# Kernel optimization log

Measured on AMD Instinct MI355X. Metric: run time of the kernel, lower is better.

The kernel has to match this reference:

```python
import jax, jax.numpy as jnp
import numpy as np

N = 8192
F_IN = 512
F_OUT = 256
NEG_SLOPE = 0.01  # F.leaky_relu default
MASK_VAL = -1000000000000000.0


def setup_inputs() -> dict:
    key = jax.random.key(0)
    k1, k2, k3, k4 = jax.random.split(key, 4)
    stdv = 1.0 / np.sqrt(F_OUT)
    x = jax.random.normal(k1, (N, F_IN), dtype=jnp.float32)
    weight = jax.random.uniform(k2, (F_IN, F_OUT), dtype=jnp.float32, minval=-stdv, maxval=stdv)
    att_vec = jax.random.normal(k3, (2 * F_OUT, 1), dtype=jnp.float32) * 0.05
    adj = jax.random.randint(k4, (N, N), 0, 2, dtype=jnp.int32)
    return {"x": x, "weight": weight, "att_vec": att_vec, "adj": adj}


def _pair_indices(n):
    # Reproduces the (buggy-but-faithful) torch.cat(dim=0).view(n,-1,2f) indexing:
    # element (i,j,:f)  = out[idx(2m)], element (i,j,f:) = out[idx(2m+1)], m = i*n+j
    # idx(r) = r // n if r < n*n else (r - n*n) % n
    nn_ = n * n
    m = jnp.arange(nn_, dtype=jnp.int32)
    r0 = 2 * m
    r1 = r0 + 1
    idx1 = jnp.where(r0 < nn_, r0 // n, (r0 - nn_) % n)
    idx2 = jnp.where(r1 < nn_, r1 // n, (r1 - nn_) % n)
    return idx1, idx2


def reference(x, weight, att_vec, adj):
    n = x.shape[0]
    f = weight.shape[1]
    # dropout p=0.0 -> identity
    out = x @ weight                      # (n, f)
    a1 = att_vec[:f, 0]                   # (f,)
    a2 = att_vec[f:, 0]                   # (f,)
    s1 = out @ a1                         # (n,)
    s2 = out @ a2                         # (n,)
    idx1, idx2 = _pair_indices(n)
    scores = (s1[idx1] + s2[idx2]).reshape(n, n)
    scores = jax.nn.leaky_relu(scores, NEG_SLOPE)
    scores = jnp.where(adj > 0, scores, MASK_VAL)
    attn = jax.nn.softmax(scores, axis=1)  # F.softmax default dim=1 for 2D
    return jax.nn.sigmoid(attn @ out)      # (n, f)
```

## Files before the change

### kernel.cpp

```cpp
#include <hip/hip_runtime.h>

using u32 = unsigned int;
using u16 = unsigned short;

typedef __attribute__((ext_vector_type(8)))  __bf16 bf16x8;
typedef __attribute__((ext_vector_type(16))) float  f32x16;
typedef __attribute__((ext_vector_type(4)))  float  f32x4;
typedef __attribute__((ext_vector_type(4)))  int    i32x4;

__device__ __forceinline__ u32 f2bf(float f){
  u32 u = __float_as_uint(f);
  return (u + 0x7FFFu + ((u >> 16) & 1u)) >> 16;
}
__device__ __forceinline__ u32 pack2bf(float lo, float hi){
  return f2bf(lo) | (f2bf(hi) << 16);
}
__device__ __forceinline__ float bfu2f(u32 us){ return __uint_as_float(us << 16); }
__device__ __forceinline__ float lrelu(float x){ return x > 0.f ? x : 0.01f * x; }

__global__ void k0_wt(const float* __restrict__ w, u16* __restrict__ wT){
  int u = blockIdx.x * 256 + threadIdx.x;
  int k = u >> 8, n = u & 255;
  wT[(size_t)n * 512 + k] = (u16)f2bf(w[(size_t)k * 256 + n]);
}

__global__ __launch_bounds__(512, 2) void k1_gemm(const float* __restrict__ x,
    const u16* __restrict__ wT, const float* __restrict__ av, u16* __restrict__ outF,
    float* __restrict__ v0, float* __restrict__ v1, u16* __restrict__ pbf){
  __shared__ float tb[8][32][36];
  __shared__ float afl[512];
  __shared__ float sred[2][32][17];
  __shared__ float srw[2][32];
  const int i0 = blockIdx.x * 32;
  const int tid = threadIdx.x;
  const int lane = tid & 63, wv = tid >> 6;
  const int r = lane & 31, h = lane >> 5;
  const float* xp = x + (size_t)(i0 + r) * 512 + h * 8;
  const u16*   bp = wT + (size_t)(wv * 32 + r) * 512 + h * 8;
  f32x16 acc = {};
  for (int s = 0; s < 32; ++s){
    f32x4 a0 = *(const f32x4*)xp;
    f32x4 a1 = *(const f32x4*)(xp + 4);
    i32x4 pk = { (int)pack2bf(a0[0], a0[1]), (int)pack2bf(a0[2], a0[3]),
                 (int)pack2bf(a1[0], a1[1]), (int)pack2bf(a1[2], a1[3]) };
    bf16x8 af = __builtin_bit_cast(bf16x8, pk);
    bf16x8 bf = *(const bf16x8*)bp;
    acc = __builtin_amdgcn_mfma_f32_32x32x16_bf16(af, bf, acc, 0, 0, 0);
    xp += 16; bp += 16;
  }
  #pragma unroll
  for (int re = 0; re < 16; ++re){
    int rr = (re & 3) + 8 * (re >> 2) + 4 * h;
    tb[wv][r][rr] = acc[re];
  }
  afl[tid] = av[tid];
  __syncthreads();
  {
    const int n2 = lane >> 1, ic = (lane & 1) * 16;
    const float* tp = &tb[wv][n2][ic];
    i32x4 w0 = { (int)pack2bf(tp[0],tp[1]),   (int)pack2bf(tp[2],tp[3]),
                 (int)pack2bf(tp[4],tp[5]),   (int)pack2bf(tp[6],tp[7]) };
    i32x4 w1 = { (int)pack2bf(tp[8],tp[9]),   (int)pack2bf(tp[10],tp[11]),
                 (int)pack2bf(tp[12],tp[13]), (int)pack2bf(tp[14],tp[15]) };
    const int n = wv * 32 + n2;
    const int k16 = (i0 + ic) >> 4;
    u16* op = outF + ((size_t)k16 * 256 + n) * 16;
    *(i32x4*)op = w0;
    *((i32x4*)op + 1) = w1;
  }
  const int row = tid & 31, g = tid >> 5;
  const int w8 = g >> 1, fh = (g & 1) * 16;
  float a1c = 0.f, a2c = 0.f;
  #pragma unroll
  for (int f = 0; f < 16; ++f){
    float tv = tb[w8][fh + f][row];
    a1c = fmaf(tv, afl[w8 * 32 + fh + f], a1c);
    a2c = fmaf(tv, afl[256 + w8 * 32 + fh + f], a2c);
  }
  sred[0][row][g] = a1c; sred[1][row][g] = a2c;
  __syncthreads();
  if (tid < 64){
    int which = tid >> 5, r2 = tid & 31;
    float s = 0.f;
    #pragma unroll
    for (int g2 = 0; g2 < 16; ++g2) s += sred[which][r2][g2];
    srw[which][r2] = s;
  }
  __syncthreads();
  if (tid < 16){
    int k = (i0 >> 1) + tid;
    float sa  = srw[0][2*tid],   sb  = srw[1][2*tid];
    float sa1 = srw[0][2*tid+1], sb1 = srw[1][2*tid+1];
    v0[k] = lrelu(sa + sb);
    v1[k] = lrelu(sa1 + sb1);
    float w = lrelu(sa + sb1);
    pbf[k] = (u16)f2bf(__expf(w));
  }
}

__global__ __launch_bounds__(512, 2) void k3_main(const int* __restrict__ adj,
    const u16* __restrict__ outF, const u16* __restrict__ pbf,
    float* __restrict__ P, float* __restrict__ pd){
  __shared__ u16 AbS[2][16896];
  __shared__ u32 plS[2048];
  __shared__ float dshS[32];
  const int bid = blockIdx.x;
  const int xcd = bid & 7, slot = bid >> 3;
  const int c = xcd & 1;
  const int tile = (xcd >> 1) * 64 + slot;
  const bool top = tile < 128;
  const int i0 = tile * 32;
  const int pb = tile * 2 + c;
  const int tid = threadIdx.x, l = tid & 63, w = tid >> 6;
  const int r = l & 31, h = l >> 5;
  const int fb = w * 32;
  const int* aq0 = adj + (size_t)(i0 + w) * 8192 + c * 4096 + l * 4;
  const u16* bq0 = outF + (size_t)c * 1048576 + (fb + r) * 16 + h * 8;

  if (top){
    plS[tid] = 0x3F803F80u; plS[tid + 512] = 0x3F803F80u;
    plS[tid + 1024] = 0x3F803F80u; plS[tid + 1536] = 0x3F803F80u;
  } else {
    const u32* ps = (const u32*)pbf;
    plS[tid] = ps[tid]; plS[tid + 512] = ps[tid + 512];
    plS[tid + 1024] = ps[tid + 1024]; plS[tid + 1536] = ps[tid + 1536];
  }
  __syncthreads();

  i32x4 ar[8];
  bf16x8 BA[4], BB[4];
  f32x16 acc = {};
  float d4[4] = {0.f, 0.f, 0.f, 0.f};

#define ADJ_H(HF_,PH_) { \
  _Pragma("unroll") for (int j_ = 0; j_ < 2; ++j_){ \
    const int q_ = (HF_) * 2 + j_; \
    const int* ap_ = aq0 + q_ * 65536 + (PH_) * 512; \
    ar[q_*2]   = *(const i32x4*)ap_; \
    ar[q_*2+1] = *(const i32x4*)(ap_ + 256); } \
  asm volatile("" ::: "memory"); }

#define B_ISS4(B_,G_) { const u16* bb_ = bq0 + (size_t)(G_) * 4096; \
  B_[0] = *(const bf16x8*)bb_;            B_[1] = *(const bf16x8*)(bb_ + 4096); \
  B_[2] = *(const bf16x8*)(bb_ + 8192);   B_[3] = *(const bf16x8*)(bb_ + 12288); \
  asm volatile("" ::: "memory"); }

#define MFMA4(B_,RB_,S_) { \
  __builtin_amdgcn_s_setprio(1); \
  _Pragma("unroll") for (int j_ = 0; j_ < 4; ++j_){ \
    bf16x8 a_ = *(const bf16x8*)((RB_) + ((S_) * 4 + j_) * 528 + r * 16 + h * 8); \
    acc = __builtin_amdgcn_mfma_f32_32x32x16_bf16(a_, B_[j_], acc, 0, 0, 0); } \
  __builtin_amdgcn_s_setprio(0); }

#define PACK(PH_,WB_) { \
  _Pragma("unroll") for (int q_ = 0; q_ < 4; ++q_){ \
    const int row_ = q_ * 8 + w; \
    _Pragma("unroll") for (int L_ = 0; L_ < 2; ++L_){ \
      i32x4 a_ = ar[q_*2 + L_]; \
      uint2 pp_ = *(const uint2*)(plS + (((PH_) & 7) * 256 + L_ * 128 + 2 * l)); \
      u32 w0_ = ((((u32)(-a_[0])) & 0xFFFFu) | (((u32)(-a_[1])) << 16)) & pp_.x; \
      u32 w1_ = ((((u32)(-a_[2])) & 0xFFFFu) | (((u32)(-a_[3])) << 16)) & pp_.y; \
      d4[q_] += __uint_as_float(w0_ << 16) + __uint_as_float(w0_ & 0xFFFF0000u) \
              + __uint_as_float(w1_ << 16) + __uint_as_float(w1_ & 0xFFFF0000u); \
      const int slot_ = L_ * 16 + (l >> 2); \
      uint2 wv_; wv_.x = w0_; wv_.y = w1_; \
      *(uint2*)((WB_) + slot_ * 528 + row_ * 16 + (l & 3) * 4) = wv_; } } }

#define KBAR() { asm volatile("s_waitcnt lgkmcnt(0)" ::: "memory"); \
  __builtin_amdgcn_s_barrier(); asm volatile("" ::: "memory"); }

  ADJ_H(0, 0); ADJ_H(1, 0);
  B_ISS4(BA, 0);
  PACK(0, &AbS[0][0]);
  KBAR();

  #pragma unroll 1
  for (int t = 0; t < 8; ++t){
    const u16* rb = &AbS[t & 1][0];
    u16* wb = &AbS[(t + 1) & 1][0];
    #pragma unroll
    for (int s = 0; s < 8; ++s){
      if (!(t == 7 && s == 7)){
        const int g = t * 32 + (s + 1) * 4;
        if (s & 1){ B_ISS4(BA, g); } else { B_ISS4(BB, g); }
      }
      if (t < 7 && s == 0) ADJ_H(0, t + 1);
      if (t < 7 && s == 1) ADJ_H(1, t + 1);
      if (s & 1){ MFMA4(BB, rb, s); } else { MFMA4(BA, rb, s); }
    }
    if (t < 7){
      PACK(t + 1, wb);
      KBAR();
    }
  }

#undef ADJ_H
#undef B_ISS4
#undef MFMA4
#undef PACK
#undef KBAR

  #pragma unroll
  for (int q = 0; q < 4; ++q){
    float v = d4[q];
    #pragma unroll
    for (int mk = 1; mk < 64; mk <<= 1) v += __shfl_xor(v, mk);
    if (l == 0) dshS[q * 8 + w] = v;
  }
  __syncthreads();
  if (tid < 32) pd[(size_t)pb * 32 + tid] = dshS[tid];
  float* Pb = P + (size_t)pb * 8192 + fb + r;
  #pragma unroll
  for (int e = 0; e < 16; ++e){
    int rr = (e & 3) + 8 * (e >> 2) + 4 * h;
    __builtin_nontemporal_store(acc[e], Pb + (size_t)rr * 256);
  }
}

__global__ void k4_final(const float* __restrict__ P, const float* __restrict__ pd,
    const float* __restrict__ v0, const float* __restrict__ v1, float* __restrict__ out){
  const int i = blockIdx.x, n = threadIdx.x;
  const int tile = i >> 5, rloc = i & 31;
  const size_t base = (size_t)tile * 16384 + (size_t)rloc * 256 + n;
  float P0 = __builtin_nontemporal_load(P + base);
  float P1 = __builtin_nontemporal_load(P + base + 8192);
  float d0 = pd[tile * 64 + rloc];
  float d1 = pd[tile * 64 + 32 + rloc];
  float val;
  if (i < 4096){
    float va = v0[i], vb = v1[i];
    float m = fmaxf(va, vb);
    float e0 = __expf(va - m), e1 = __expf(vb - m);
    val = (e0 * P0 + e1 * P1) / (e0 * d0 + e1 * d1);
  } else {
    val = (P0 + P1) / (d0 + d1);
  }
  out[(size_t)i * 256 + n] = 1.0f / (1.0f + __expf(-val));
}

extern "C" void kernel_launch(void* const* d_in, const int* in_sizes, int n_in,
                              void* d_out, int out_size, void* d_ws, size_t ws_size,
                              hipStream_t stream)
{
  const float* x      = (const float*)d_in[0];
  const float* weight = (const float*)d_in[1];
  const float* av     = (const float*)d_in[2];
  const int*   adj    = (const int*)d_in[3];
  float* out = (float*)d_out;
  char* ws = (char*)d_ws;
  float* P     = (float*)(ws + 0);
  float* pd    = (float*)(ws + 16777216);
  u16*   outF  = (u16*)  (ws + 16842752);
  u16*   wT    = (u16*)  (ws + 21037056);
  u16*   pbf   = (u16*)  (ws + 21299200);
  float* v0    = (float*)(ws + 21307392);
  float* v1    = (float*)(ws + 21323776);

  k0_wt    <<<512, 256, 0, stream>>>(weight, wT);
  k1_gemm  <<<256, 512, 0, stream>>>(x, wT, av, outF, v0, v1, pbf);
  k3_main  <<<512, 512, 0, stream>>>(adj, outF, pbf, P, pd);
  k4_final <<<8192, 256, 0, stream>>>(P, pd, v0, v1, out);
}
```

Baseline: 115.6 us.

## Warp-specialize attention kernel into adj producers and MFMA consumers with 64-row tiles

Splits each k3_main block into four producer waves that load and pack adjacency masks into LDS and four consumer waves that stream outF and run MFMAs. The row tile doubles to 64 with 2x2 MFMA accumulators per consumer wave, and the grid halves to 256 blocks with one block per CU. The aim is to overlap the adj HBM stream with matrix math and to reuse each B fragment across more rows. The risks are lower occupancy and a barrier every phase, which couples producer and consumer progress.

```diff
diff --git a/kernel.cpp b/kernel.cpp
--- a/kernel.cpp
+++ b/kernel.cpp
@@ -98,134 +98,142 @@
   }
 }
 
-__global__ __launch_bounds__(512, 2) void k3_main(const int* __restrict__ adj,
+__global__ __launch_bounds__(512, 1) void k3_main(const int* __restrict__ adj,
     const u16* __restrict__ outF, const u16* __restrict__ pbf,
     float* __restrict__ P, float* __restrict__ pd){
-  __shared__ u16 AbS[2][16896];
+  __shared__ u16 AbS[2][16768];
   __shared__ u32 plS[2048];
-  __shared__ float dshS[32];
   const int bid = blockIdx.x;
-  const int xcd = bid & 7, slot = bid >> 3;
-  const int c = xcd & 1;
-  const int tile = (xcd >> 1) * 64 + slot;
-  const bool top = tile < 128;
-  const int i0 = tile * 32;
+  const int xcd = bid & 7, grp = bid >> 3;
+  const int half = xcd & 1, c = (xcd >> 1) & 1, hi = xcd >> 2;
+  const int tile = half * 64 + hi * 32 + grp;
+  const bool top = (half == 0);
+  const int i0 = tile * 64;
+  const int kbase = c * 4096;
   const int pb = tile * 2 + c;
   const int tid = threadIdx.x, l = tid & 63, w = tid >> 6;
   const int r = l & 31, h = l >> 5;
-  const int fb = w * 32;
-  const int* aq0 = adj + (size_t)(i0 + w) * 8192 + c * 4096 + l * 4;
-  const u16* bq0 = outF + (size_t)c * 1048576 + (fb + r) * 16 + h * 8;
+  const bool isProd = (w < 4);
+  const int w4 = w & 3;
 
   if (top){
-    plS[tid] = 0x3F803F80u; plS[tid + 512] = 0x3F803F80u;
+    plS[tid] = 0x3F803F80u;        plS[tid + 512] = 0x3F803F80u;
     plS[tid + 1024] = 0x3F803F80u; plS[tid + 1536] = 0x3F803F80u;
   } else {
     const u32* ps = (const u32*)pbf;
-    plS[tid] = ps[tid]; plS[tid + 512] = ps[tid + 512];
+    plS[tid] = ps[tid];             plS[tid + 512] = ps[tid + 512];
     plS[tid + 1024] = ps[tid + 1024]; plS[tid + 1536] = ps[tid + 1536];
   }
   __syncthreads();
 
-  i32x4 ar[8];
-  bf16x8 BA[4], BB[4];
-  f32x16 acc = {};
-  float d4[4] = {0.f, 0.f, 0.f, 0.f};
-
-#define ADJ_H(HF_,PH_) { \
-  _Pragma("unroll") for (int j_ = 0; j_ < 2; ++j_){ \
-    const int q_ = (HF_) * 2 + j_; \
-    const int* ap_ = aq0 + q_ * 65536 + (PH_) * 512; \
-    ar[q_*2]   = *(const i32x4*)ap_; \
-    ar[q_*2+1] = *(const i32x4*)(ap_ + 256); } \
+  const int* aq0 = adj + (size_t)(i0 + w4 * 16) * 8192 + kbase + l * 4;
+  u16* const wp0 = &AbS[0][0] + (l >> 2) * 1048 + ((l >> 1) & 1) * 512
+                   + 4 * (l & 1) + w4 * 128;
+  const int fb = w4 * 64;
+  const u16* bq0 = outF + (size_t)c * 1048576 + (fb + r) * 16 + h * 8;
+
+  i32x4 ar[16];
+  float dd[16] = {0.f,0.f,0.f,0.f,0.f,0.f,0.f,0.f,0.f,0.f,0.f,0.f,0.f,0.f,0.f,0.f};
+  bf16x8 BA[8], BB[8];
+  f32x16 a00 = {}, a01 = {}, a10 = {}, a11 = {};
+
+#define ISSUE(T_) { _Pragma("unroll") for (int j_ = 0; j_ < 16; ++j_) \
+    ar[j_] = *(const i32x4*)(aq0 + (size_t)j_ * 8192 + (T_) * 256); \
   asm volatile("" ::: "memory"); }
 
-#define B_ISS4(B_,G_) { const u16* bb_ = bq0 + (size_t)(G_) * 4096; \
-  B_[0] = *(const bf16x8*)bb_;            B_[1] = *(const bf16x8*)(bb_ + 4096); \
-  B_[2] = *(const bf16x8*)(bb_ + 8192);   B_[3] = *(const bf16x8*)(bb_ + 12288); \
+#define BFS(W_) (__uint_as_float((W_) << 16) + __uint_as_float((W_) & 0xFFFF0000u))
+
+#define PACKALL(T_,BUF_) { \
+  u32 pp0_ = plS[(T_) * 128 + 2 * l]; \
+  u32 pp1_ = plS[(T_) * 128 + 2 * l + 1]; \
+  u16* wb_ = wp0 + (BUF_) * 16768; \
+  _Pragma("unroll") for (int j_ = 0; j_ < 16; ++j_){ \
+    i32x4 a_ = ar[j_]; \
+    u32 w0_ = ((((u32)(-a_[0])) & 0xFFFFu) | (((u32)(-a_[1])) << 16)) & pp0_; \
+    u32 w1_ = ((((u32)(-a_[2])) & 0xFFFFu) | (((u32)(-a_[3])) << 16)) & pp1_; \
+    dd[j_] += BFS(w0_) + BFS(w1_); \
+    uint2 wv_; wv_.x = w0_; wv_.y = w1_; \
+    *(uint2*)(wb_ + j_ * 8) = wv_; } }
+
+#define B_ISS(B_,G_) { const u16* bb_ = bq0 + (size_t)(G_) * 4096; \
+  _Pragma("unroll") for (int j_ = 0; j_ < 4; ++j_){ \
+    B_[2*j_]   = *(const bf16x8*)(bb_ + j_ * 4096); \
+    B_[2*j_+1] = *(const bf16x8*)(bb_ + j_ * 4096 + 512); } \
   asm volatile("" ::: "memory"); }
 
-#define MFMA4(B_,RB_,S_) { \
+#define MFMA4(B_,BUF_,S0_) { \
+  const u16* rb_ = &AbS[0][0] + (BUF_) * 16768 + (S0_) * 1048 + h * 512 + r * 8; \
   __builtin_amdgcn_s_setprio(1); \
   _Pragma("unroll") for (int j_ = 0; j_ < 4; ++j_){ \
-    bf16x8 a_ = *(const bf16x8*)((RB_) + ((S_) * 4 + j_) * 528 + r * 16 + h * 8); \
-    acc = __builtin_amdgcn_mfma_f32_32x32x16_bf16(a_, B_[j_], acc, 0, 0, 0); } \
+    bf16x8 a0_ = *(const bf16x8*)(rb_ + j_ * 1048); \
+    bf16x8 a1_ = *(const bf16x8*)(rb_ + j_ * 1048 + 256); \
+    a00 = __builtin_amdgcn_mfma_f32_32x32x16_bf16(a0_, B_[2*j_],   a00, 0, 0, 0); \
+    a01 = __builtin_amdgcn_mfma_f32_32x32x16_bf16(a0_, B_[2*j_+1], a01, 0, 0, 0); \
+    a10 = __builtin_amdgcn_mfma_f32_32x32x16_bf16(a1_, B_[2*j_],   a10, 0, 0, 0); \
+    a11 = __builtin_amdgcn_mfma_f32_32x32x16_bf16(a1_, B_[2*j_+1], a11, 0, 0, 0); } \
   __builtin_amdgcn_s_setprio(0); }
-
-#define PACK(PH_,WB_) { \
-  _Pragma("unroll") for (int q_ = 0; q_ < 4; ++q_){ \
-    const int row_ = q_ * 8 + w; \
-    _Pragma("unroll") for (int L_ = 0; L_ < 2; ++L_){ \
-      i32x4 a_ = ar[q_*2 + L_]; \
-      uint2 pp_ = *(const uint2*)(plS + (((PH_) & 7) * 256 + L_ * 128 + 2 * l)); \
-      u32 w0_ = ((((u32)(-a_[0])) & 0xFFFFu) | (((u32)(-a_[1])) << 16)) & pp_.x; \
-      u32 w1_ = ((((u32)(-a_[2])) & 0xFFFFu) | (((u32)(-a_[3])) << 16)) & pp_.y; \
-      d4[q_] += __uint_as_float(w0_ << 16) + __uint_as_float(w0_ & 0xFFFF0000u) \
-              + __uint_as_float(w1_ << 16) + __uint_as_float(w1_ & 0xFFFF0000u); \
-      const int slot_ = L_ * 16 + (l >> 2); \
-      uint2 wv_; wv_.x = w0_; wv_.y = w1_; \
-      *(uint2*)((WB_) + slot_ * 528 + row_ * 16 + (l & 3) * 4) = wv_; } } }
 
 #define KBAR() { asm volatile("s_waitcnt lgkmcnt(0)" ::: "memory"); \
   __builtin_amdgcn_s_barrier(); asm volatile("" ::: "memory"); }
 
-  ADJ_H(0, 0); ADJ_H(1, 0);
-  B_ISS4(BA, 0);
-  PACK(0, &AbS[0][0]);
-  KBAR();
-
+  if (isProd){ ISSUE(0); } else { B_ISS(BA, 0); }
   #pragma unroll 1
-  for (int t = 0; t < 8; ++t){
-    const u16* rb = &AbS[t & 1][0];
-    u16* wb = &AbS[(t + 1) & 1][0];
+  for (int t = 0; t <= 16; ++t){
+    if (isProd){
+      if (t < 16){
+        PACKALL(t, t & 1);
+        if (t < 15) ISSUE(t + 1);
+      }
+    } else {
+      if (t >= 1){
+        const int ph = t - 1, buf = ph & 1, g0 = ph * 16;
+        B_ISS(BB, g0 + 4);  MFMA4(BA, buf, 0);
+        B_ISS(BA, g0 + 8);  MFMA4(BB, buf, 4);
+        B_ISS(BB, g0 + 12); MFMA4(BA, buf, 8);
+        if (ph < 15){ B_ISS(BA, g0 + 16); }
+        MFMA4(BB, buf, 12);
+      }
+    }
+    KBAR();
+  }
+
+#undef ISSUE
+#undef PACKALL
+#undef B_ISS
+#undef MFMA4
+#undef KBAR
+#undef BFS
+
+  if (isProd){
     #pragma unroll
-    for (int s = 0; s < 8; ++s){
-      if (!(t == 7 && s == 7)){
-        const int g = t * 32 + (s + 1) * 4;
-        if (s & 1){ B_ISS4(BA, g); } else { B_ISS4(BB, g); }
-      }
-      if (t < 7 && s == 0) ADJ_H(0, t + 1);
-      if (t < 7 && s == 1) ADJ_H(1, t + 1);
-      if (s & 1){ MFMA4(BB, rb, s); } else { MFMA4(BA, rb, s); }
+    for (int j = 0; j < 16; ++j){
+      float v = dd[j];
+      #pragma unroll
+      for (int mk = 1; mk < 64; mk <<= 1) v += __shfl_xor(v, mk);
+      if (l == 0) pd[(size_t)pb * 64 + w4 * 16 + j] = v;
     }
-    if (t < 7){
-      PACK(t + 1, wb);
-      KBAR();
+  } else {
+    float* Pb = P + (size_t)pb * 16384 + fb + r;
+    #pragma unroll
+    for (int e = 0; e < 16; ++e){
+      int rr = (e & 3) + 8 * (e >> 2) + 4 * h;
+      __builtin_nontemporal_store(a00[e], Pb + (size_t)rr * 256);
+      __builtin_nontemporal_store(a01[e], Pb + (size_t)rr * 256 + 32);
+      __builtin_nontemporal_store(a10[e], Pb + (size_t)(rr + 32) * 256);
+      __builtin_nontemporal_store(a11[e], Pb + (size_t)(rr + 32) * 256 + 32);
     }
-  }
-
-#undef ADJ_H
-#undef B_ISS4
-#undef MFMA4
-#undef PACK
-#undef KBAR
-
-  #pragma unroll
-  for (int q = 0; q < 4; ++q){
-    float v = d4[q];
-    #pragma unroll
-    for (int mk = 1; mk < 64; mk <<= 1) v += __shfl_xor(v, mk);
-    if (l == 0) dshS[q * 8 + w] = v;
-  }
-  __syncthreads();
-  if (tid < 32) pd[(size_t)pb * 32 + tid] = dshS[tid];
-  float* Pb = P + (size_t)pb * 8192 + fb + r;
-  #pragma unroll
-  for (int e = 0; e < 16; ++e){
-    int rr = (e & 3) + 8 * (e >> 2) + 4 * h;
-    __builtin_nontemporal_store(acc[e], Pb + (size_t)rr * 256);
   }
 }
 
 __global__ void k4_final(const float* __restrict__ P, const float* __restrict__ pd,
     const float* __restrict__ v0, const float* __restrict__ v1, float* __restrict__ out){
   const int i = blockIdx.x, n = threadIdx.x;
-  const int tile = i >> 5, rloc = i & 31;
-  const size_t base = (size_t)tile * 16384 + (size_t)rloc * 256 + n;
+  const int tile = i >> 6, rloc = i & 63;
+  const size_t base = (size_t)(tile * 2) * 16384 + (size_t)rloc * 256 + n;
   float P0 = __builtin_nontemporal_load(P + base);
-  float P1 = __builtin_nontemporal_load(P + base + 8192);
-  float d0 = pd[tile * 64 + rloc];
-  float d1 = pd[tile * 64 + 32 + rloc];
+  float P1 = __builtin_nontemporal_load(P + base + 16384);
+  float d0 = pd[tile * 128 + rloc];
+  float d1 = pd[tile * 128 + 64 + rloc];
   float val;
   if (i < 4096){
     float va = v0[i], vb = v1[i];
@@ -256,8 +264,8 @@
   float* v0    = (float*)(ws + 21307392);
   float* v1    = (float*)(ws + 21323776);
 
-  k0_wt    <<<512, 256, 0, stream>>>(weight, wT);
-  k1_gemm  <<<256, 512, 0, stream>>>(x, wT, av, outF, v0, v1, pbf);
-  k3_main  <<<512, 512, 0, stream>>>(adj, outF, pbf, P, pd);
-  k4_final <<<8192, 256, 0, stream>>>(P, pd, v0, v1, out);
-}
+  k0_wt   <<<512, 256, 0, stream>>>(weight, wT);
+  k1_gemm <<<256, 512, 0, stream>>>(x, wT, av, outF, v0, v1, pbf);
+  k3_main <<<256, 512, 0, stream>>>(adj, outF, pbf, P, pd);
+  k4_final<<<8192, 256, 0, stream>>>(P, pd, v0, v1, out);
+}
```

Measured after the change: 105.3 us. -8.9%, faster.
